# Kernel tuning notes

Hardware: AMD Instinct MI355X
Metric: run time of the kernel (lower is better)

Reference implementation:

```python
import jax, jax.numpy as jnp
import numpy as np

NEG_SLOPE = 0.2  # PyG GATConv default negative_slope


def setup_inputs() -> dict:
    key = jax.random.key(0)
    k1, k2, k3, k4, k5 = jax.random.split(key, 5)
    N, E, IN, H, C = 50000, 800000, 128, 4, 64
    x = jax.random.normal(k1, (N, IN), dtype=jnp.float32)
    edge_index = jax.random.randint(k2, (2, E), 0, N, dtype=jnp.int32)
    W = jax.random.normal(k3, (IN, H * C), dtype=jnp.float32) * (1.0 / np.sqrt(IN))
    att_src = jax.random.normal(k4, (H, C), dtype=jnp.float32) * 0.1
    att_dst = jax.random.normal(k5, (H, C), dtype=jnp.float32) * 0.1
    bias = jnp.zeros((C,), dtype=jnp.float32)
    return {"x": x, "edge_index": edge_index, "W": W,
            "att_src": att_src, "att_dst": att_dst, "bias": bias}


def reference(x, edge_index, W, att_src, att_dst, bias):
    N = x.shape[0]
    H, C = att_src.shape
    # add self loops (PyG GATConv default add_self_loops=True)
    loop = jnp.arange(N, dtype=edge_index.dtype)
    src = jnp.concatenate([edge_index[0], loop])  # message source j
    dst = jnp.concatenate([edge_index[1], loop])  # message target i
    # linear projection, per-head view [N, H, C]
    h = (x @ W).reshape(N, H, C)
    # per-node attention terms [N, H]
    a_src = jnp.einsum('nhc,hc->nh', h, att_src)
    a_dst = jnp.einsum('nhc,hc->nh', h, att_dst)
    # per-edge logits with leaky relu [Etot, H]
    e = jax.nn.leaky_relu(a_src[src] + a_dst[dst], NEG_SLOPE)
    # segment softmax over incoming edges of each destination node
    emax = jax.ops.segment_max(e, dst, num_segments=N)       # [N, H]
    ex = jnp.exp(e - emax[dst])                              # [Etot, H]
    denom = jax.ops.segment_sum(ex, dst, num_segments=N)     # [N, H]
    alpha = ex / denom[dst]                                  # [Etot, H]
    # weighted scatter-aggregate of source features
    msg = h[src] * alpha[:, :, None]                         # [Etot, H, C]
    out = jax.ops.segment_sum(msg, dst, num_segments=N)      # [N, H, C]
    # concat=False -> mean over heads, then bias, then module-level ELU
    out = out.mean(axis=1) + bias
    return jax.nn.elu(out)
```

## Files before the change

### kernel.cpp

```cpp
#include <hip/hip_runtime.h>

#define NEG_SLOPE 0.2f
static constexpr int IN_F = 128;
static constexpr int NHEAD = 4;
static constexpr int CH = 64;
static constexpr int HC = 256;

static __host__ size_t align256(size_t v) { return (v + 255) & ~((size_t)255); }

__device__ inline ushort f2bf(float f) {
    unsigned u = __float_as_uint(f);
    unsigned r = u + 0x7FFFu + ((u >> 16) & 1u);
    return (ushort)(r >> 16);
}
__device__ inline float bf2f(ushort s) { return __uint_as_float(((unsigned)s) << 16); }

typedef short s16x8 __attribute__((ext_vector_type(8)));
typedef float f32x16 __attribute__((ext_vector_type(16)));

__global__ __launch_bounds__(256) void gemm_mfma_kernel(
    const float* __restrict__ x, const float* __restrict__ W,
    const float* __restrict__ att_src, const float* __restrict__ att_dst,
    ushort* __restrict__ hb, float* __restrict__ a_src, float* __restrict__ a_dst,
    int* __restrict__ coarse_cnt, int NB, int N)
{
    constexpr int LDK = 136;
    constexpr int HS  = 72;
    __shared__ ushort As[64 * LDK];
    __shared__ ushort Bs[64 * LDK];
    ushort* Hs = As;

    const int t = threadIdx.x;
    const int m0 = blockIdx.x * 64;
    const int head = blockIdx.y;
    const int n0 = head * 64;

    if (blockIdx.x == 0 && blockIdx.y == 0 && t < NB) coarse_cnt[t] = 0;

    #pragma unroll
    for (int u = 0; u < 8; ++u) {
        int f = t + 256 * u;
        int r = f >> 5;
        int c4 = (f & 31) * 4;
        int row = m0 + r;
        float4 v = make_float4(0.f, 0.f, 0.f, 0.f);
        if (row < N) v = *(const float4*)(x + (size_t)row * IN_F + c4);
        ushort4 o;
        o.x = f2bf(v.x); o.y = f2bf(v.y); o.z = f2bf(v.z); o.w = f2bf(v.w);
        *(ushort4*)&As[r * LDK + c4] = o;
    }
    #pragma unroll
    for (int u = 0; u < 8; ++u) {
        int f = t + 256 * u;
        int k = f >> 4;
        int n4 = (f & 15) * 4;
        float4 v = *(const float4*)(W + (size_t)k * HC + n0 + n4);
        Bs[(n4 + 0) * LDK + k] = f2bf(v.x);
        Bs[(n4 + 1) * LDK + k] = f2bf(v.y);
        Bs[(n4 + 2) * LDK + k] = f2bf(v.z);
        Bs[(n4 + 3) * LDK + k] = f2bf(v.w);
    }
    __syncthreads();

    const int w = t >> 6;
    const int lane = t & 63;
    const int mbase = 32 * (w >> 1) + (lane & 31);
    const int nbase = 32 * (w & 1) + (lane & 31);
    const int kq = (lane >> 5) * 8;

    f32x16 acc = {};
    #pragma unroll
    for (int s = 0; s < 8; ++s) {
        s16x8 af = *(const s16x8*)&As[mbase * LDK + 16 * s + kq];
        s16x8 bf = *(const s16x8*)&Bs[nbase * LDK + 16 * s + kq];
        acc = __builtin_amdgcn_mfma_f32_32x32x16_bf16(af, bf, acc, 0, 0, 0);
    }
    __syncthreads();

    {
        int colL = (lane & 31) + 32 * (w & 1);
        int rbase = 4 * (lane >> 5) + 32 * (w >> 1);
        #pragma unroll
        for (int r = 0; r < 16; ++r) {
            int rowL = rbase + (r & 3) + 8 * (r >> 2);
            Hs[rowL * HS + colL] = f2bf(acc[r]);
        }
    }
    __syncthreads();

    {
        int r2 = t >> 2;
        int q = t & 3;
        int row = m0 + r2;
        uint4 p0 = *(const uint4*)&Hs[r2 * HS + 16 * q];
        uint4 p1 = *(const uint4*)&Hs[r2 * HS + 16 * q + 8];
        if (row < N) {
            *(uint4*)(hb + (size_t)row * HC + n0 + 16 * q) = p0;
            *(uint4*)(hb + (size_t)row * HC + n0 + 16 * q + 8) = p1;
        }
        const float* asp = att_src + n0 + 16 * q;
        const float* adp = att_dst + n0 + 16 * q;
        unsigned uu[8] = { p0.x, p0.y, p0.z, p0.w, p1.x, p1.y, p1.z, p1.w };
        float ps = 0.f, pd = 0.f;
        #pragma unroll
        for (int i = 0; i < 8; ++i) {
            float lo = bf2f((ushort)(uu[i] & 0xFFFFu));
            float hi = bf2f((ushort)(uu[i] >> 16));
            ps += lo * asp[2 * i] + hi * asp[2 * i + 1];
            pd += lo * adp[2 * i] + hi * adp[2 * i + 1];
        }
        ps += __shfl_xor(ps, 1, 64); ps += __shfl_xor(ps, 2, 64);
        pd += __shfl_xor(pd, 1, 64); pd += __shfl_xor(pd, 2, 64);
        if (q == 0 && row < N) {
            a_src[(size_t)row * NHEAD + head] = ps;
            a_dst[(size_t)row * NHEAD + head] = pd;
        }
    }
}


__global__ __launch_bounds__(256) void bucket_count(
    const int* __restrict__ dst, int* __restrict__ coarse_cnt,
    int E, int epb, int NB)
{
    __shared__ int hist[256];
    int t = threadIdx.x;
    hist[t] = 0;
    __syncthreads();
    int lo = blockIdx.x * epb;
    int hi = min(E, lo + epb);
    for (int i = lo + t; i < hi; i += 256)
        atomicAdd(&hist[((unsigned)dst[i]) >> 8], 1);
    __syncthreads();
    if (t < NB && hist[t]) atomicAdd(&coarse_cnt[t], hist[t]);
}

__global__ __launch_bounds__(256) void scan_coarse(
    const int* __restrict__ coarse_cnt, int* __restrict__ ebase,
    int* __restrict__ bucket_cur, int* __restrict__ rowptr,
    int NB, int N, int E)
{
    __shared__ int sm[256];
    int t = threadIdx.x;
    int v = (t < NB) ? coarse_cnt[t] : 0;
    sm[t] = v;
    __syncthreads();
    #pragma unroll
    for (int off = 1; off < 256; off <<= 1) {
        int a = sm[t];
        int b = (t >= off) ? sm[t - off] : 0;
        __syncthreads();
        sm[t] = a + b;
        __syncthreads();
    }
    int incl = sm[t];
    int excl = incl - v;
    if (t < NB) { ebase[t] = excl; bucket_cur[t] = excl; }
    if (t == NB - 1) ebase[NB] = incl;
    if (t == 0) rowptr[N] = E + N;
}

__global__ __launch_bounds__(256) void bucket_scatter(
    const int* __restrict__ src, const int* __restrict__ dst,
    int* __restrict__ bucket_cur, unsigned* __restrict__ ebuf,
    int E, int epb, int NB)
{
    __shared__ int hist[256];
    __shared__ int base[256];
    int t = threadIdx.x;
    hist[t] = 0;
    __syncthreads();
    int lo = blockIdx.x * epb;
    int hi = min(E, lo + epb);
    for (int i = lo + t; i < hi; i += 256)
        atomicAdd(&hist[((unsigned)dst[i]) >> 8], 1);
    __syncthreads();
    if (t < NB && hist[t]) base[t] = atomicAdd(&bucket_cur[t], hist[t]);
    __syncthreads();
    hist[t] = 0;
    __syncthreads();
    for (int i = lo + t; i < hi; i += 256) {
        unsigned d = (unsigned)dst[i];
        unsigned b = d >> 8;
        int off2 = atomicAdd(&hist[b], 1);
        ebuf[base[b] + off2] = (((unsigned)src[i]) << 8) | (d & 255u);
    }
}

__global__ __launch_bounds__(256) void csr_build(
    const unsigned* __restrict__ ebuf, const int* __restrict__ ebase,
    int* __restrict__ rowptr, int* __restrict__ csr_src, int N)
{
    __shared__ int hist[256];
    __shared__ int scn[256];
    __shared__ int cur[256];
    int b = blockIdx.x;
    int t = threadIdx.x;
    int n0 = b << 8;
    int ncnt = min(256, N - n0);
    int lo = ebase[b], hi = ebase[b + 1];
    int cb = lo + n0;
    hist[t] = 0;
    __syncthreads();
    for (int i = lo + t; i < hi; i += 256)
        atomicAdd(&hist[ebuf[i] & 255u], 1);
    __syncthreads();
    int v = hist[t];
    scn[t] = v;
    __syncthreads();
    #pragma unroll
    for (int off = 1; off < 256; off <<= 1) {
        int a = scn[t];
        int bb = (t >= off) ? scn[t - off] : 0;
        __syncthreads();
        scn[t] = a + bb;
        __syncthreads();
    }
    int excl = scn[t] - v;
    int segstart = cb + excl + t;
    if (t < ncnt) {
        rowptr[n0 + t] = segstart;
        csr_src[segstart] = n0 + t;
    }
    cur[t] = excl + t + 1;
    __syncthreads();
    for (int i = lo + t; i < hi; i += 256) {
        unsigned e = ebuf[i];
        int ln = (int)(e & 255u);
        int pos = atomicAdd(&cur[ln], 1);
        csr_src[cb + pos] = (int)(e >> 8);
    }
}

__global__ __launch_bounds__(256) void aggregate_kernel(
    const ushort* __restrict__ hb, const float* __restrict__ a_src,
    const float* __restrict__ a_dst, const int* __restrict__ rowptr,
    const int* __restrict__ csr_src, const float* __restrict__ bias,
    float* __restrict__ out, int N)
{
    int node = (int)((blockIdx.x * (size_t)blockDim.x + threadIdx.x) >> 6);
    int l = threadIdx.x & 63;
    if (node >= N) return;
    int start = rowptr[node];
    int end = rowptr[node + 1];
    int hd = l >> 4;
    float adh = a_dst[(size_t)node * NHEAD + hd];

    float4 acc0 = make_float4(0.f, 0.f, 0.f, 0.f);
    float4 acc1 = make_float4(0.f, 0.f, 0.f, 0.f);
    float4 acc2 = make_float4(0.f, 0.f, 0.f, 0.f);
    float4 acc3 = make_float4(0.f, 0.f, 0.f, 0.f);
    float s0 = 0.f, s1 = 0.f, s2 = 0.f, s3 = 0.f;

    int k = start;
    for (; k + 4 <= end; k += 4) {
        int sj0 = csr_src[k];
        int sj1 = csr_src[k + 1];
        int sj2 = csr_src[k + 2];
        int sj3 = csr_src[k + 3];
        float a0 = a_src[(size_t)sj0 * NHEAD + hd];
        float a1 = a_src[(size_t)sj1 * NHEAD + hd];
        float a2 = a_src[(size_t)sj2 * NHEAD + hd];
        float a3 = a_src[(size_t)sj3 * NHEAD + hd];
        ushort4 h0 = *(const ushort4*)(hb + ((size_t)sj0 << 8) + 4 * l);
        ushort4 h1 = *(const ushort4*)(hb + ((size_t)sj1 << 8) + 4 * l);
        ushort4 h2 = *(const ushort4*)(hb + ((size_t)sj2 << 8) + 4 * l);
        ushort4 h3 = *(const ushort4*)(hb + ((size_t)sj3 << 8) + 4 * l);
        float e0 = a0 + adh; e0 = fmaxf(e0, NEG_SLOPE * e0); float w0 = __expf(e0);
        float e1 = a1 + adh; e1 = fmaxf(e1, NEG_SLOPE * e1); float w1 = __expf(e1);
        float e2 = a2 + adh; e2 = fmaxf(e2, NEG_SLOPE * e2); float w2 = __expf(e2);
        float e3 = a3 + adh; e3 = fmaxf(e3, NEG_SLOPE * e3); float w3 = __expf(e3);
        s0 += w0; s1 += w1; s2 += w2; s3 += w3;
        acc0.x += w0 * bf2f(h0.x); acc0.y += w0 * bf2f(h0.y);
        acc0.z += w0 * bf2f(h0.z); acc0.w += w0 * bf2f(h0.w);
        acc1.x += w1 * bf2f(h1.x); acc1.y += w1 * bf2f(h1.y);
        acc1.z += w1 * bf2f(h1.z); acc1.w += w1 * bf2f(h1.w);
        acc2.x += w2 * bf2f(h2.x); acc2.y += w2 * bf2f(h2.y);
        acc2.z += w2 * bf2f(h2.z); acc2.w += w2 * bf2f(h2.w);
        acc3.x += w3 * bf2f(h3.x); acc3.y += w3 * bf2f(h3.y);
        acc3.z += w3 * bf2f(h3.z); acc3.w += w3 * bf2f(h3.w);
    }
    for (; k < end; ++k) {
        int sj0 = csr_src[k];
        float a0 = a_src[(size_t)sj0 * NHEAD + hd];
        ushort4 h0 = *(const ushort4*)(hb + ((size_t)sj0 << 8) + 4 * l);
        float e0 = a0 + adh; e0 = fmaxf(e0, NEG_SLOPE * e0);
        float w0 = __expf(e0);
        s0 += w0;
        acc0.x += w0 * bf2f(h0.x); acc0.y += w0 * bf2f(h0.y);
        acc0.z += w0 * bf2f(h0.z); acc0.w += w0 * bf2f(h0.w);
    }

    float inv = 1.0f / (s0 + s1 + s2 + s3);
    float4 acc;
    acc.x = (acc0.x + acc1.x + acc2.x + acc3.x) * inv;
    acc.y = (acc0.y + acc1.y + acc2.y + acc3.y) * inv;
    acc.z = (acc0.z + acc1.z + acc2.z + acc3.z) * inv;
    acc.w = (acc0.w + acc1.w + acc2.w + acc3.w) * inv;

    #pragma unroll
    for (int off = 16; off < 64; off <<= 1) {
        acc.x += __shfl_xor(acc.x, off, 64);
        acc.y += __shfl_xor(acc.y, off, 64);
        acc.z += __shfl_xor(acc.z, off, 64);
        acc.w += __shfl_xor(acc.w, off, 64);
    }
    if (l < 16) {
        float4 b4 = *(const float4*)(bias + 4 * l);
        float4 o;
        o.x = acc.x * 0.25f + b4.x;
        o.y = acc.y * 0.25f + b4.y;
        o.z = acc.z * 0.25f + b4.z;
        o.w = acc.w * 0.25f + b4.w;
        o.x = (o.x > 0.f) ? o.x : (__expf(o.x) - 1.f);
        o.y = (o.y > 0.f) ? o.y : (__expf(o.y) - 1.f);
        o.z = (o.z > 0.f) ? o.z : (__expf(o.z) - 1.f);
        o.w = (o.w > 0.f) ? o.w : (__expf(o.w) - 1.f);
        *(float4*)(out + (size_t)node * CH + 4 * l) = o;
    }
}

extern "C" void kernel_launch(void* const* d_in, const int* in_sizes, int n_in,
                              void* d_out, int out_size, void* d_ws, size_t ws_size,
                              hipStream_t stream)
{
    const float* x         = (const float*)d_in[0];
    const int*   edge_idx  = (const int*)d_in[1];
    const float* W         = (const float*)d_in[2];
    const float* att_src   = (const float*)d_in[3];
    const float* att_dst   = (const float*)d_in[4];
    const float* bias      = (const float*)d_in[5];
    float* out = (float*)d_out;

    const int N = in_sizes[0] / IN_F;
    const int E = in_sizes[1] / 2;
    const int Etot = E + N;
    const int NB = (N + 255) >> 8;
    const int* srcp = edge_idx;
    const int* dstp = edge_idx + E;

    char* ws = (char*)d_ws;
    size_t off = 0;
    ushort*  hb     = (ushort*)(ws + off);   off += align256((size_t)N * HC * sizeof(ushort));
    float*   a_src  = (float*)(ws + off);    off += align256((size_t)N * NHEAD * sizeof(float));
    float*   a_dst  = (float*)(ws + off);    off += align256((size_t)N * NHEAD * sizeof(float));
    int*     ccnt   = (int*)(ws + off);      off += align256(256 * sizeof(int));
    int*     ebase  = (int*)(ws + off);      off += align256(257 * sizeof(int));
    int*     bcur   = (int*)(ws + off);      off += align256(256 * sizeof(int));
    unsigned* ebuf  = (unsigned*)(ws + off); off += align256((size_t)E * sizeof(unsigned));
    int*     rowptr = (int*)(ws + off);      off += align256(((size_t)N + 1) * sizeof(int));
    int*     csrs   = (int*)(ws + off);      off += align256((size_t)Etot * sizeof(int));
    (void)ws_size; (void)n_in; (void)out_size;

    const int PB = 416;
    const int epb = (E + PB - 1) / PB;

    dim3 gg((N + 63) / 64, NHEAD);
    gemm_mfma_kernel<<<gg, 256, 0, stream>>>(x, W, att_src, att_dst, hb,
                                             a_src, a_dst, ccnt, NB, N);
    bucket_count<<<PB, 256, 0, stream>>>(dstp, ccnt, E, epb, NB);
    scan_coarse<<<1, 256, 0, stream>>>(ccnt, ebase, bcur, rowptr, NB, N, E);
    bucket_scatter<<<PB, 256, 0, stream>>>(srcp, dstp, bcur, ebuf, E, epb, NB);
    csr_build<<<NB, 256, 0, stream>>>(ebuf, ebase, rowptr, csrs, N);
    aggregate_kernel<<<((size_t)N * 64 + 255) / 256, 256, 0, stream>>>(
        hb, a_src, a_dst, rowptr, csrs, bias, out, N);
}
```

Measured before the change: 214.1 us.

## Fuse bucket count into GEMM grid, pretranspose W, widen GEMM tile, unroll aggregation

New measurement: 210.1 us. About the same (-1.9%).

```diff
diff --git a/kernel.cpp b/kernel.cpp
--- a/kernel.cpp
+++ b/kernel.cpp
@@ -18,72 +18,95 @@
 typedef short s16x8 __attribute__((ext_vector_type(8)));
 typedef float f32x16 __attribute__((ext_vector_type(16)));
 
+__global__ __launch_bounds__(256) void prep_kernel(
+    const float* __restrict__ W, ushort* __restrict__ Wt,
+    int* __restrict__ coarse_cnt)
+{
+    int f = blockIdx.x * 256 + threadIdx.x;
+    int k = f >> 8;
+    int n = f & 255;
+    Wt[n * IN_F + k] = f2bf(W[(size_t)k * HC + n]);
+    if (blockIdx.x == 0) coarse_cnt[threadIdx.x] = 0;
+}
+
 __global__ __launch_bounds__(256) void gemm_mfma_kernel(
-    const float* __restrict__ x, const float* __restrict__ W,
+    const float* __restrict__ x, const ushort* __restrict__ Wt,
     const float* __restrict__ att_src, const float* __restrict__ att_dst,
     ushort* __restrict__ hb, float* __restrict__ a_src, float* __restrict__ a_dst,
-    int* __restrict__ coarse_cnt, int NB, int N)
+    const int* __restrict__ dst, int* __restrict__ coarse_cnt,
+    int E, int epb, int NTB, int NB, int N)
 {
     constexpr int LDK = 136;
-    constexpr int HS  = 72;
     __shared__ ushort As[64 * LDK];
-    __shared__ ushort Bs[64 * LDK];
+    __shared__ ushort Bs[128 * LDK];
     ushort* Hs = As;
 
     const int t = threadIdx.x;
+
+    if (blockIdx.x >= NTB) {
+        int* hist = (int*)As;
+        hist[t] = 0;
+        __syncthreads();
+        int slice = (blockIdx.x - NTB) * 2 + blockIdx.y;
+        int lo = slice * epb;
+        int hi = min(E, lo + epb);
+        for (int i = lo + t; i < hi; i += 256)
+            atomicAdd(&hist[((unsigned)dst[i]) >> 8], 1);
+        __syncthreads();
+        if (t < NB && hist[t]) atomicAdd(&coarse_cnt[t], hist[t]);
+        return;
+    }
+
     const int m0 = blockIdx.x * 64;
-    const int head = blockIdx.y;
-    const int n0 = head * 64;
-
-    if (blockIdx.x == 0 && blockIdx.y == 0 && t < NB) coarse_cnt[t] = 0;
+    const int n0 = blockIdx.y * 128;
 
     #pragma unroll
     for (int u = 0; u < 8; ++u) {
         int f = t + 256 * u;
         int r = f >> 5;
-        int c4 = (f & 31) * 4;
+        int k4 = (f & 31) * 4;
         int row = m0 + r;
         float4 v = make_float4(0.f, 0.f, 0.f, 0.f);
-        if (row < N) v = *(const float4*)(x + (size_t)row * IN_F + c4);
+        if (row < N) v = *(const float4*)(x + (size_t)row * IN_F + k4);
         ushort4 o;
         o.x = f2bf(v.x); o.y = f2bf(v.y); o.z = f2bf(v.z); o.w = f2bf(v.w);
-        *(ushort4*)&As[r * LDK + c4] = o;
+        *(ushort4*)&As[r * LDK + k4] = o;
     }
     #pragma unroll
     for (int u = 0; u < 8; ++u) {
         int f = t + 256 * u;
-        int k = f >> 4;
-        int n4 = (f & 15) * 4;
-        float4 v = *(const float4*)(W + (size_t)k * HC + n0 + n4);
-        Bs[(n4 + 0) * LDK + k] = f2bf(v.x);
-        Bs[(n4 + 1) * LDK + k] = f2bf(v.y);
-        Bs[(n4 + 2) * LDK + k] = f2bf(v.z);
-        Bs[(n4 + 3) * LDK + k] = f2bf(v.w);
+        int n = f >> 4;
+        int k8 = (f & 15) * 8;
+        uint4 v = *(const uint4*)(Wt + (size_t)(n0 + n) * IN_F + k8);
+        *(uint4*)&Bs[n * LDK + k8] = v;
     }
     __syncthreads();
 
     const int w = t >> 6;
     const int lane = t & 63;
-    const int mbase = 32 * (w >> 1) + (lane & 31);
-    const int nbase = 32 * (w & 1) + (lane & 31);
+    const int mrow = 32 * (w >> 1) + (lane & 31);
+    const int nbase = 64 * (w & 1) + (lane & 31);
     const int kq = (lane >> 5) * 8;
 
-    f32x16 acc = {};
+    f32x16 acc0 = {}, acc1 = {};
     #pragma unroll
     for (int s = 0; s < 8; ++s) {
-        s16x8 af = *(const s16x8*)&As[mbase * LDK + 16 * s + kq];
-        s16x8 bf = *(const s16x8*)&Bs[nbase * LDK + 16 * s + kq];
-        acc = __builtin_amdgcn_mfma_f32_32x32x16_bf16(af, bf, acc, 0, 0, 0);
+        s16x8 af = *(const s16x8*)&As[mrow * LDK + 16 * s + kq];
+        s16x8 b0 = *(const s16x8*)&Bs[nbase * LDK + 16 * s + kq];
+        s16x8 b1 = *(const s16x8*)&Bs[(nbase + 32) * LDK + 16 * s + kq];
+        acc0 = __builtin_amdgcn_mfma_f32_32x32x16_bf16(af, b0, acc0, 0, 0, 0);
+        acc1 = __builtin_amdgcn_mfma_f32_32x32x16_bf16(af, b1, acc1, 0, 0, 0);
     }
     __syncthreads();
 
     {
-        int colL = (lane & 31) + 32 * (w & 1);
         int rbase = 4 * (lane >> 5) + 32 * (w >> 1);
+        int c0 = 64 * (w & 1) + (lane & 31);
         #pragma unroll
         for (int r = 0; r < 16; ++r) {
             int rowL = rbase + (r & 3) + 8 * (r >> 2);
-            Hs[rowL * HS + colL] = f2bf(acc[r]);
+            Hs[rowL * LDK + c0]      = f2bf(acc0[r]);
+            Hs[rowL * LDK + c0 + 32] = f2bf(acc1[r]);
         }
     }
     __syncthreads();
@@ -92,47 +115,38 @@
         int r2 = t >> 2;
         int q = t & 3;
         int row = m0 + r2;
-        uint4 p0 = *(const uint4*)&Hs[r2 * HS + 16 * q];
-        uint4 p1 = *(const uint4*)&Hs[r2 * HS + 16 * q + 8];
+        uint4 p0 = *(const uint4*)&Hs[r2 * LDK + 32 * q];
+        uint4 p1 = *(const uint4*)&Hs[r2 * LDK + 32 * q + 8];
+        uint4 p2 = *(const uint4*)&Hs[r2 * LDK + 32 * q + 16];
+        uint4 p3 = *(const uint4*)&Hs[r2 * LDK + 32 * q + 24];
         if (row < N) {
-            *(uint4*)(hb + (size_t)row * HC + n0 + 16 * q) = p0;
-            *(uint4*)(hb + (size_t)row * HC + n0 + 16 * q + 8) = p1;
-        }
-        const float* asp = att_src + n0 + 16 * q;
-        const float* adp = att_dst + n0 + 16 * q;
-        unsigned uu[8] = { p0.x, p0.y, p0.z, p0.w, p1.x, p1.y, p1.z, p1.w };
+            ushort* dsth = hb + (size_t)row * HC + n0 + 32 * q;
+            *(uint4*)(dsth)      = p0;
+            *(uint4*)(dsth + 8)  = p1;
+            *(uint4*)(dsth + 16) = p2;
+            *(uint4*)(dsth + 24) = p3;
+        }
+        int hq = 2 * blockIdx.y + (q >> 1);
+        int cb = (q & 1) * 32;
+        const float* asp = att_src + hq * CH + cb;
+        const float* adp = att_dst + hq * CH + cb;
+        unsigned uu[16] = { p0.x, p0.y, p0.z, p0.w, p1.x, p1.y, p1.z, p1.w,
+                            p2.x, p2.y, p2.z, p2.w, p3.x, p3.y, p3.z, p3.w };
         float ps = 0.f, pd = 0.f;
         #pragma unroll
-        for (int i = 0; i < 8; ++i) {
+        for (int i = 0; i < 16; ++i) {
             float lo = bf2f((ushort)(uu[i] & 0xFFFFu));
             float hi = bf2f((ushort)(uu[i] >> 16));
             ps += lo * asp[2 * i] + hi * asp[2 * i + 1];
             pd += lo * adp[2 * i] + hi * adp[2 * i + 1];
         }
-        ps += __shfl_xor(ps, 1, 64); ps += __shfl_xor(ps, 2, 64);
-        pd += __shfl_xor(pd, 1, 64); pd += __shfl_xor(pd, 2, 64);
-        if (q == 0 && row < N) {
-            a_src[(size_t)row * NHEAD + head] = ps;
-            a_dst[(size_t)row * NHEAD + head] = pd;
-        }
-    }
-}
-
-
-__global__ __launch_bounds__(256) void bucket_count(
-    const int* __restrict__ dst, int* __restrict__ coarse_cnt,
-    int E, int epb, int NB)
-{
-    __shared__ int hist[256];
-    int t = threadIdx.x;
-    hist[t] = 0;
-    __syncthreads();
-    int lo = blockIdx.x * epb;
-    int hi = min(E, lo + epb);
-    for (int i = lo + t; i < hi; i += 256)
-        atomicAdd(&hist[((unsigned)dst[i]) >> 8], 1);
-    __syncthreads();
-    if (t < NB && hist[t]) atomicAdd(&coarse_cnt[t], hist[t]);
+        ps += __shfl_xor(ps, 1, 64);
+        pd += __shfl_xor(pd, 1, 64);
+        if ((q & 1) == 0 && row < N) {
+            a_src[(size_t)row * NHEAD + hq] = ps;
+            a_dst[(size_t)row * NHEAD + hq] = pd;
+        }
+    }
 }
 
 __global__ __launch_bounds__(256) void scan_coarse(
@@ -246,39 +260,50 @@
     int hd = l >> 4;
     float adh = a_dst[(size_t)node * NHEAD + hd];
 
-    float4 acc0 = make_float4(0.f, 0.f, 0.f, 0.f);
-    float4 acc1 = make_float4(0.f, 0.f, 0.f, 0.f);
-    float4 acc2 = make_float4(0.f, 0.f, 0.f, 0.f);
-    float4 acc3 = make_float4(0.f, 0.f, 0.f, 0.f);
-    float s0 = 0.f, s1 = 0.f, s2 = 0.f, s3 = 0.f;
+    float4 acc[4];
+    float s[4];
+    #pragma unroll
+    for (int u = 0; u < 4; ++u) { acc[u] = make_float4(0.f,0.f,0.f,0.f); s[u] = 0.f; }
 
     int k = start;
+    for (; k + 8 <= end; k += 8) {
+        int sj[8];
+        #pragma unroll
+        for (int u = 0; u < 8; ++u) sj[u] = csr_src[k + u];
+        float av[8]; ushort4 hv[8];
+        #pragma unroll
+        for (int u = 0; u < 8; ++u) {
+            av[u] = a_src[(size_t)sj[u] * NHEAD + hd];
+            hv[u] = *(const ushort4*)(hb + ((size_t)sj[u] << 8) + 4 * l);
+        }
+        #pragma unroll
+        for (int u = 0; u < 8; ++u) {
+            float e = av[u] + adh; e = fmaxf(e, NEG_SLOPE * e);
+            float wgt = __expf(e);
+            int q = u & 3;
+            s[q] += wgt;
+            acc[q].x += wgt * bf2f(hv[u].x); acc[q].y += wgt * bf2f(hv[u].y);
+            acc[q].z += wgt * bf2f(hv[u].z); acc[q].w += wgt * bf2f(hv[u].w);
+        }
+    }
     for (; k + 4 <= end; k += 4) {
-        int sj0 = csr_src[k];
-        int sj1 = csr_src[k + 1];
-        int sj2 = csr_src[k + 2];
-        int sj3 = csr_src[k + 3];
-        float a0 = a_src[(size_t)sj0 * NHEAD + hd];
-        float a1 = a_src[(size_t)sj1 * NHEAD + hd];
-        float a2 = a_src[(size_t)sj2 * NHEAD + hd];
-        float a3 = a_src[(size_t)sj3 * NHEAD + hd];
-        ushort4 h0 = *(const ushort4*)(hb + ((size_t)sj0 << 8) + 4 * l);
-        ushort4 h1 = *(const ushort4*)(hb + ((size_t)sj1 << 8) + 4 * l);
-        ushort4 h2 = *(const ushort4*)(hb + ((size_t)sj2 << 8) + 4 * l);
-        ushort4 h3 = *(const ushort4*)(hb + ((size_t)sj3 << 8) + 4 * l);
-        float e0 = a0 + adh; e0 = fmaxf(e0, NEG_SLOPE * e0); float w0 = __expf(e0);
-        float e1 = a1 + adh; e1 = fmaxf(e1, NEG_SLOPE * e1); float w1 = __expf(e1);
-        float e2 = a2 + adh; e2 = fmaxf(e2, NEG_SLOPE * e2); float w2 = __expf(e2);
-        float e3 = a3 + adh; e3 = fmaxf(e3, NEG_SLOPE * e3); float w3 = __expf(e3);
-        s0 += w0; s1 += w1; s2 += w2; s3 += w3;
-        acc0.x += w0 * bf2f(h0.x); acc0.y += w0 * bf2f(h0.y);
-        acc0.z += w0 * bf2f(h0.z); acc0.w += w0 * bf2f(h0.w);
-        acc1.x += w1 * bf2f(h1.x); acc1.y += w1 * bf2f(h1.y);
-        acc1.z += w1 * bf2f(h1.z); acc1.w += w1 * bf2f(h1.w);
-        acc2.x += w2 * bf2f(h2.x); acc2.y += w2 * bf2f(h2.y);
-        acc2.z += w2 * bf2f(h2.z); acc2.w += w2 * bf2f(h2.w);
-        acc3.x += w3 * bf2f(h3.x); acc3.y += w3 * bf2f(h3.y);
-        acc3.z += w3 * bf2f(h3.z); acc3.w += w3 * bf2f(h3.w);
+        int sj[4];
+        #pragma unroll
+        for (int u = 0; u < 4; ++u) sj[u] = csr_src[k + u];
+        float av[4]; ushort4 hv[4];
+        #pragma unroll
+        for (int u = 0; u < 4; ++u) {
+            av[u] = a_src[(size_t)sj[u] * NHEAD + hd];
+            hv[u] = *(const ushort4*)(hb + ((size_t)sj[u] << 8) + 4 * l);
+        }
+        #pragma unroll
+        for (int u = 0; u < 4; ++u) {
+            float e = av[u] + adh; e = fmaxf(e, NEG_SLOPE * e);
+            float wgt = __expf(e);
+            s[u] += wgt;
+            acc[u].x += wgt * bf2f(hv[u].x); acc[u].y += wgt * bf2f(hv[u].y);
+            acc[u].z += wgt * bf2f(hv[u].z); acc[u].w += wgt * bf2f(hv[u].w);
+        }
     }
     for (; k < end; ++k) {
         int sj0 = csr_src[k];
@@ -286,32 +311,32 @@
         ushort4 h0 = *(const ushort4*)(hb + ((size_t)sj0 << 8) + 4 * l);
         float e0 = a0 + adh; e0 = fmaxf(e0, NEG_SLOPE * e0);
         float w0 = __expf(e0);
-        s0 += w0;
-        acc0.x += w0 * bf2f(h0.x); acc0.y += w0 * bf2f(h0.y);
-        acc0.z += w0 * bf2f(h0.z); acc0.w += w0 * bf2f(h0.w);
-    }
-
-    float inv = 1.0f / (s0 + s1 + s2 + s3);
-    float4 acc;
-    acc.x = (acc0.x + acc1.x + acc2.x + acc3.x) * inv;
-    acc.y = (acc0.y + acc1.y + acc2.y + acc3.y) * inv;
-    acc.z = (acc0.z + acc1.z + acc2.z + acc3.z) * inv;
-    acc.w = (acc0.w + acc1.w + acc2.w + acc3.w) * inv;
+        s[0] += w0;
+        acc[0].x += w0 * bf2f(h0.x); acc[0].y += w0 * bf2f(h0.y);
+        acc[0].z += w0 * bf2f(h0.z); acc[0].w += w0 * bf2f(h0.w);
+    }
+
+    float inv = 1.0f / (s[0] + s[1] + s[2] + s[3]);
+    float4 a4;
+    a4.x = (acc[0].x + acc[1].x + acc[2].x + acc[3].x) * inv;
+    a4.y = (acc[0].y + acc[1].y + acc[2].y + acc[3].y) * inv;
+    a4.z = (acc[0].z + acc[1].z + acc[2].z + acc[3].z) * inv;
+    a4.w = (acc[0].w + acc[1].w + acc[2].w + acc[3].w) * inv;
 
     #pragma unroll
     for (int off = 16; off < 64; off <<= 1) {
-        acc.x += __shfl_xor(acc.x, off, 64);
-        acc.y += __shfl_xor(acc.y, off, 64);
-        acc.z += __shfl_xor(acc.z, off, 64);
-        acc.w += __shfl_xor(acc.w, off, 64);
+        a4.x += __shfl_xor(a4.x, off, 64);
+        a4.y += __shfl_xor(a4.y, off, 64);
+        a4.z += __shfl_xor(a4.z, off, 64);
+        a4.w += __shfl_xor(a4.w, off, 64);
     }
     if (l < 16) {
         float4 b4 = *(const float4*)(bias + 4 * l);
         float4 o;
-        o.x = acc.x * 0.25f + b4.x;
-        o.y = acc.y * 0.25f + b4.y;
-        o.z = acc.z * 0.25f + b4.z;
-        o.w = acc.w * 0.25f + b4.w;
+        o.x = a4.x * 0.25f + b4.x;
+        o.y = a4.y * 0.25f + b4.y;
+        o.z = a4.z * 0.25f + b4.z;
+        o.w = a4.w * 0.25f + b4.w;
         o.x = (o.x > 0.f) ? o.x : (__expf(o.x) - 1.f);
         o.y = (o.y > 0.f) ? o.y : (__expf(o.y) - 1.f);
         o.z = (o.z > 0.f) ? o.z : (__expf(o.z) - 1.f);
@@ -342,6 +367,7 @@
     char* ws = (char*)d_ws;
     size_t off = 0;
     ushort*  hb     = (ushort*)(ws + off);   off += align256((size_t)N * HC * sizeof(ushort));
+    ushort*  Wt     = (ushort*)(ws + off);   off += align256((size_t)HC * IN_F * sizeof(ushort));
     float*   a_src  = (float*)(ws + off);    off += align256((size_t)N * NHEAD * sizeof(float));
     float*   a_dst  = (float*)(ws + off);    off += align256((size_t)N * NHEAD * sizeof(float));
     int*     ccnt   = (int*)(ws + off);      off += align256(256 * sizeof(int));
@@ -352,13 +378,17 @@
     int*     csrs   = (int*)(ws + off);      off += align256((size_t)Etot * sizeof(int));
     (void)ws_size; (void)n_in; (void)out_size;
 
+    const int NTB = (N + 63) / 64;
+    const int PBC = 208;
+    const int epbc = (E + 2 * PBC - 1) / (2 * PBC);
     const int PB = 416;
     const int epb = (E + PB - 1) / PB;
 
-    dim3 gg((N + 63) / 64, NHEAD);
-    gemm_mfma_kernel<<<gg, 256, 0, stream>>>(x, W, att_src, att_dst, hb,
-                                             a_src, a_dst, ccnt, NB, N);
-    bucket_count<<<PB, 256, 0, stream>>>(dstp, ccnt, E, epb, NB);
+    prep_kernel<<<IN_F * HC / 256, 256, 0, stream>>>(W, Wt, ccnt);
+    dim3 gg(NTB + PBC, 2);
+    gemm_mfma_kernel<<<gg, 256, 0, stream>>>(x, Wt, att_src, att_dst, hb,
+                                             a_src, a_dst, dstp, ccnt,
+                                             E, epbc, NTB, NB, N);
     scan_coarse<<<1, 256, 0, stream>>>(ccnt, ebase, bcur, rowptr, NB, N, E);
     bucket_scatter<<<PB, 256, 0, stream>>>(srcp, dstp, bcur, ebuf, E, epb, NB);
     csr_build<<<NB, 256, 0, stream>>>(ebuf, ebase, rowptr, csrs, N);
```
